# Performance work log

Hardware: AMD Instinct MI355X
Metric: run time of the kernel (lower is better)

Reference implementation:

```python
import jax, jax.numpy as jnp
import numpy as np

NEG_INF = -9e15  # matches torch's -9000000000000000.0 mask value
ALPHA = 0.2      # LeakyReLU negative slope


def setup_inputs() -> dict:
    key = jax.random.key(0)
    k1, k2, k3, k4 = jax.random.split(key, 4)
    B, N, Fin, Fout = 8, 2048, 256, 256
    h = jax.random.normal(k1, (B, N, Fin), dtype=jnp.float32)
    adj = jax.random.randint(k2, (B, N, N), 0, 2, dtype=jnp.int32)
    # xavier_uniform with gain=1.414
    limW = 1.414 * np.sqrt(6.0 / (Fin + Fout))
    W = jax.random.uniform(k3, (Fin, Fout), minval=-limW, maxval=limW, dtype=jnp.float32)
    lima = 1.414 * np.sqrt(6.0 / (2 * Fout + 1))
    a = jax.random.uniform(k4, (2 * Fout, 1), minval=-lima, maxval=lima, dtype=jnp.float32)
    return {"h": h, "adj": adj, "W": W, "a": a}


def reference(h, adj, W, a):
    # h: (B, N, Fin), adj: (B, N, N), W: (Fin, Fout), a: (2*Fout, 1)
    Fout = W.shape[1]
    Wh = jnp.einsum('bni,io->bno', h, W)                 # (B, N, Fout)
    # e[b,i,j] = leakyrelu(Wh[b,i] @ a1 + Wh[b,j] @ a2) -- equivalent to the
    # original concat([Wh_i, Wh_j]) @ a without the O(N^2 * 2F) intermediate.
    e1 = Wh @ a[:Fout, 0]                                # (B, N)
    e2 = Wh @ a[Fout:, 0]                                # (B, N)
    e = jax.nn.leaky_relu(e1[:, :, None] + e2[:, None, :], negative_slope=ALPHA)
    masked = jnp.where(adj > 0, e, NEG_INF)
    attention = jax.nn.softmax(masked, axis=-1)          # (B, N, N)
    # dropout omitted (deterministic eval-mode reference)
    h_prime = jnp.einsum('bij,bjo->bio', attention, Wh)  # (B, N, Fout)
    return jax.nn.elu(h_prime), attention
```

## Files before the change

### kernel.cpp

```cpp
#include <hip/hip_runtime.h>
#include <hip/hip_bf16.h>
#include <stdint.h>

#define NEG_INF -9.0e15f
#define LRELU_ALPHA 0.2f
#define LOG2E 1.442695040888963f

using bf16x8  = __attribute__((ext_vector_type(8))) short;
using f32x4   = __attribute__((ext_vector_type(4))) float;
using short4v = __attribute__((ext_vector_type(4))) short;
using int4v   = __attribute__((ext_vector_type(4))) int;
using float4v = __attribute__((ext_vector_type(4))) float;
using uint4v  = __attribute__((ext_vector_type(4))) unsigned;

static __device__ __forceinline__ float b2f(short s) {
  unsigned u = ((unsigned)(unsigned short)s) << 16;
  return __builtin_bit_cast(float, u);
}
static __device__ __forceinline__ short f2bf(float f) {
  unsigned u = __builtin_bit_cast(unsigned, f);
  u = u + 0x7FFFu + ((u >> 16) & 1u);
  return (short)(u >> 16);
}
static __device__ __forceinline__ unsigned cvtpk_bf16(float lo, float hi) {
  unsigned r;
  asm volatile("v_cvt_pk_bf16_f32 %0, %1, %2" : "=v"(r) : "v"(lo), "v"(hi));
  return r;
}
static __device__ __forceinline__ void gload16(const void* g, void* l) {
  __builtin_amdgcn_global_load_lds((const __attribute__((address_space(1))) void*)g,
                                   (__attribute__((address_space(3))) void*)l, 16, 0, 0);
}

__global__ __launch_bounds__(256) void castT_W_kernel(
    const float* __restrict__ src, short* __restrict__ dst)
{
  __shared__ float t[64][65];
  const int m0 = blockIdx.x * 64, n0 = blockIdx.y * 64;
  const int tid = threadIdx.x;
  const int rr = tid >> 3, cc = (tid & 7) * 8;
#pragma unroll
  for (int p = 0; p < 2; ++p) {
    int row = rr + p * 32;
    const float* sp = src + (m0 + row) * 256 + n0 + cc;
    float4v v0 = *(const float4v*)sp;
    float4v v1 = *(const float4v*)(sp + 4);
#pragma unroll
    for (int j = 0; j < 4; ++j) { t[row][cc + j] = v0[j]; t[row][cc + 4 + j] = v1[j]; }
  }
  __syncthreads();
#pragma unroll
  for (int p = 0; p < 2; ++p) {
    int orow = rr + p * 32;
    short vv[8] __attribute__((aligned(16)));
#pragma unroll
    for (int j = 0; j < 8; ++j) vv[j] = f2bf(t[cc + j][orow]);
    short* dp = dst + (n0 + orow) * 256 + m0 + cc;
    *(int4v*)dp = *(const int4v*)vv;
  }
}

__global__ __launch_bounds__(256) void transpose_bf16_kernel(
    const short* __restrict__ src, short* __restrict__ dst,
    int M, int N, long long ss, long long ds)
{
  __shared__ short t[64][68];
  const int b = blockIdx.z;
  src += (long long)b * ss; dst += (long long)b * ds;
  const int m0 = blockIdx.x * 64, n0 = blockIdx.y * 64;
  const int tid = threadIdx.x;
  const int rr = tid >> 3, cc = (tid & 7) * 8;
#pragma unroll
  for (int p = 0; p < 2; ++p) {
    int row = rr + p * 32;
    const short* sp = src + (long long)(m0 + row) * N + n0 + cc;
    short4v v0 = *(const short4v*)sp;
    short4v v1 = *(const short4v*)(sp + 4);
    *(short4v*)&t[row][cc]     = v0;
    *(short4v*)&t[row][cc + 4] = v1;
  }
  __syncthreads();
#pragma unroll
  for (int p = 0; p < 2; ++p) {
    int orow = rr + p * 32;
    short vv[8] __attribute__((aligned(16)));
#pragma unroll
    for (int j = 0; j < 8; ++j) vv[j] = t[cc + j][orow];
    short* dp = dst + (long long)(n0 + orow) * M + m0 + cc;
    *(int4v*)dp = *(const int4v*)vv;
  }
}

__global__ __launch_bounds__(256) void evec_kernel(
    const short* __restrict__ Wh, const float* __restrict__ a,
    float* __restrict__ e1, float* __restrict__ e2)
{
  const int wid = threadIdx.x >> 6, lane = threadIdx.x & 63;
  const long long r = (long long)blockIdx.x * 4 + wid;
  short4v hv   = *(const short4v*)(Wh + r * 256 + lane * 4);
  float4v a1v  = *(const float4v*)(a + lane * 4);
  float4v a2v  = *(const float4v*)(a + 256 + lane * 4);
  float s1 = 0.f, s2 = 0.f;
#pragma unroll
  for (int k = 0; k < 4; ++k) {
    float x = b2f(hv[k]);
    s1 += x * a1v[k];
    s2 += x * a2v[k];
  }
#pragma unroll
  for (int off = 32; off > 0; off >>= 1) {
    s1 += __shfl_xor(s1, off, 64);
    s2 += __shfl_xor(s2, off, 64);
  }
  if (lane == 0) { e1[r] = s1; e2[r] = s2; }
}

__global__ __launch_bounds__(256) void pack_stats_kernel(
    const int* __restrict__ adj, const float* __restrict__ e1,
    const float* __restrict__ e2, unsigned char* __restrict__ mask,
    float* __restrict__ Lr, float* __restrict__ Dr)
{
  const int i = blockIdx.x;
  const int b = blockIdx.y;
  const long long row = (long long)b * 2048 + i;
  const int tid = threadIdx.x;
  const int wid = tid >> 6, lane = tid & 63;
  const int j0 = tid * 8;

  const int*   arow = adj + row * 2048 + j0;
  const float  ei   = e1[row];
  const float* e2b  = e2 + b * 2048 + j0;

  int4v   a0 = *(const int4v*)(arow);
  int4v   a1 = *(const int4v*)(arow + 4);
  float4v f0 = *(const float4v*)(e2b);
  float4v f1 = *(const float4v*)(e2b + 4);

  float s[8]; unsigned byte = 0u;
#pragma unroll
  for (int k = 0; k < 8; ++k) {
    float x = ei + (k < 4 ? f0[k] : f1[k - 4]);
    float v = fmaxf(x, LRELU_ALPHA * x);
    int  ad = (k < 4 ? a0[k] : a1[k - 4]);
    if (ad > 0) { s[k] = v; byte |= (1u << k); } else s[k] = NEG_INF;
  }
  float m = s[0];
#pragma unroll
  for (int k = 1; k < 8; ++k) m = fmaxf(m, s[k]);
#pragma unroll
  for (int off = 32; off > 0; off >>= 1) m = fmaxf(m, __shfl_xor(m, off, 64));

  __shared__ float wmax[4], wsum[4];
  if (lane == 0) wmax[wid] = m;
  __syncthreads();
  const float M = fmaxf(fmaxf(wmax[0], wmax[1]), fmaxf(wmax[2], wmax[3]));
  const bool empty = (M == NEG_INF);

  mask[row * 256 + tid] = empty ? (unsigned char)0xFF : (unsigned char)byte;

  float t = 0.f;
#pragma unroll
  for (int k = 0; k < 8; ++k) t += __expf(s[k] - M);
#pragma unroll
  for (int off = 32; off > 0; off >>= 1) t += __shfl_xor(t, off, 64);
  if (lane == 0) wsum[wid] = t;
  __syncthreads();
  if (tid == 0) {
    const float S = wsum[0] + wsum[1] + wsum[2] + wsum[3];
    Lr[row] = empty ? 0.0f : LOG2E;
    Dr[row] = empty ? -11.0f : (-M * LOG2E - __log2f(S));
  }
}

__global__ __launch_bounds__(256, 2) void pv_kernel(
    const unsigned char* __restrict__ mask, const float* __restrict__ e1,
    const float* __restrict__ e2, const float* __restrict__ Lr,
    const float* __restrict__ Dr, const short* __restrict__ Bt,
    float* __restrict__ attnw, float* __restrict__ C)
{
  __shared__ short As0[32 * 64],  As1[32 * 64];
  __shared__ short Bs0[256 * 64], Bs1[256 * 64];
  const int bid = blockIdx.x;
  const int bz  = bid & 7;
  const int M0  = (bid >> 3) << 5;
  const int tid = threadIdx.x;
  const int w = tid >> 6, lane = tid & 63;
  const int g = lane >> 4, lr = lane & 15;

  const long long rb = (long long)bz * 2048;
  Bt    += (long long)bz * 524288;
  attnw += (long long)bz * 4194304;
  C     += (long long)bz * 524288;

  const int pr = tid >> 3, kc8 = tid & 7;
  const int prow = M0 + pr;
  const float E1p = e1[rb + prow];
  const float Lp  = Lr[rb + prow];
  const float Dp  = Dr[rb + prow];
  const unsigned char* mrow = mask + (rb + prow) * 256;
  float* arow = attnw + (long long)prow * 2048;
  const int as_off = pr * 64 + ((kc8 ^ (pr & 7)) << 3);
  const float* e2b = e2 + rb;

  const int bcol_off = lane >> 3;
  const int bchunk   = (lane & 7) ^ ((lane >> 3) & 7);

  f32x4 acc[2][4] = {};

  auto STAGE = [&](short* BsD, short* AsD, int k0) {
#pragma unroll
    for (int q = 0; q < 8; ++q) {
      int pp = w * 8 + q;
      int col = pp * 8 + bcol_off;
      gload16(Bt + (long long)col * 2048 + k0 + bchunk * 8, BsD + pp * 512);
    }
    const unsigned by = mrow[(k0 >> 3) + kc8];
    const int kk = k0 + kc8 * 8;
    float4v eo = *(const float4v*)(e2b + kk);
    float4v eh = *(const float4v*)(e2b + kk + 4);
    float p[8];
#pragma unroll
    for (int e = 0; e < 8; ++e) {
      float x = E1p + (e < 4 ? eo[e] : eh[e - 4]);
      float v = fmaxf(x, LRELU_ALPHA * x);
      float P = __builtin_amdgcn_exp2f(fmaf(v, Lp, Dp));
      p[e] = ((by >> e) & 1u) ? P : 0.0f;
    }
    float4v o0, o1;
#pragma unroll
    for (int e = 0; e < 4; ++e) { o0[e] = p[e]; o1[e] = p[e + 4]; }
    *(float4v*)(arow + kk)     = o0;
    *(float4v*)(arow + kk + 4) = o1;
    uint4v uv;
    uv[0] = cvtpk_bf16(p[0], p[1]);
    uv[1] = cvtpk_bf16(p[2], p[3]);
    uv[2] = cvtpk_bf16(p[4], p[5]);
    uv[3] = cvtpk_bf16(p[6], p[7]);
    *(bf16x8*)(AsD + as_off) = __builtin_bit_cast(bf16x8, uv);
  };

  auto COMPUTE = [&](const short* BsD, const short* AsD) {
    bf16x8 af[2][2], bfr[4][2];
#pragma unroll
    for (int i = 0; i < 2; ++i) {
      int row = i * 16 + lr;
#pragma unroll
      for (int s = 0; s < 2; ++s)
        af[i][s] = *(const bf16x8*)(AsD + row * 64 + (((s * 4 + g) ^ (row & 7)) << 3));
    }
#pragma unroll
    for (int j = 0; j < 4; ++j) {
      int col = w * 64 + j * 16 + lr;
#pragma unroll
      for (int s = 0; s < 2; ++s)
        bfr[j][s] = *(const bf16x8*)(BsD + col * 64 + (((s * 4 + g) ^ (col & 7)) << 3));
    }
#pragma unroll
    for (int s = 0; s < 2; ++s)
#pragma unroll
      for (int i = 0; i < 2; ++i)
#pragma unroll
        for (int j = 0; j < 4; ++j)
          acc[i][j] = __builtin_amdgcn_mfma_f32_16x16x32_bf16(af[i][s], bfr[j][s], acc[i][j], 0, 0, 0);
  };

  STAGE(Bs0, As0, 0);
  __syncthreads();
  for (int t = 0; t < 32; t += 2) {
    STAGE(Bs1, As1, (t + 1) * 64);
    COMPUTE(Bs0, As0);
    __syncthreads();
    if (t + 2 < 32) STAGE(Bs0, As0, (t + 2) * 64);
    COMPUTE(Bs1, As1);
    __syncthreads();
  }

#pragma unroll
  for (int i = 0; i < 2; ++i) {
    int row_base = M0 + i * 16 + 4 * g;
#pragma unroll
    for (int j = 0; j < 4; ++j) {
      int col = w * 64 + j * 16 + lr;
#pragma unroll
      for (int r = 0; r < 4; ++r) {
        float v = acc[i][j][r];
        v = (v > 0.f) ? v : (__expf(v) - 1.f);
        C[(long long)(row_base + r) * 256 + col] = v;
      }
    }
  }
}

__global__ __launch_bounds__(256) void gemm_h_kernel(
    const float* __restrict__ A, const short* __restrict__ Bt,
    short* __restrict__ C, int N, int K)
{
  __shared__ short As[128 * 32];
  __shared__ short Bs[128 * 32];
  const int m0 = blockIdx.x * 128, n0 = blockIdx.y * 128;
  const int tid = threadIdx.x;
  const int w = tid >> 6, lane = tid & 63;
  const int wr = w >> 1, wc = w & 1;
  const int g = lane >> 4, lr = lane & 15;

  f32x4 acc[4][4] = {};

  for (int k0 = 0; k0 < K; k0 += 32) {
    __syncthreads();
#pragma unroll
    for (int q = 0; q < 2; ++q) {
      int c = q * 256 + tid;
      int row = c >> 2, kq = (c & 3) << 3;
      const float* ap = A + (long long)(m0 + row) * K + k0 + kq;
      float4v u0 = *(const float4v*)ap;
      float4v u1 = *(const float4v*)(ap + 4);
      uint4v uv;
      uv[0] = cvtpk_bf16(u0[0], u0[1]);
      uv[1] = cvtpk_bf16(u0[2], u0[3]);
      uv[2] = cvtpk_bf16(u1[0], u1[1]);
      uv[3] = cvtpk_bf16(u1[2], u1[3]);
      *(bf16x8*)(As + c * 8) = __builtin_bit_cast(bf16x8, uv);
    }
#pragma unroll
    for (int q = 0; q < 2; ++q) {
      int p = w * 2 + q;
      int c = p * 64 + lane;
      int row = c >> 2, kq = (c & 3) << 3;
      gload16(Bt + (long long)(n0 + row) * K + k0 + kq, Bs + p * 512);
    }
    __syncthreads();

    bf16x8 af[4], bfr[4];
#pragma unroll
    for (int i = 0; i < 4; ++i) {
      af[i]  = *(const bf16x8*)(As + (wr * 64 + i * 16 + lr) * 32 + 8 * g);
      bfr[i] = *(const bf16x8*)(Bs + (wc * 64 + i * 16 + lr) * 32 + 8 * g);
    }
#pragma unroll
    for (int i = 0; i < 4; ++i)
#pragma unroll
      for (int j = 0; j < 4; ++j)
        acc[i][j] = __builtin_amdgcn_mfma_f32_16x16x32_bf16(af[i], bfr[j], acc[i][j], 0, 0, 0);
  }

#pragma unroll
  for (int i = 0; i < 4; ++i) {
    int row_base = m0 + wr * 64 + i * 16 + 4 * g;
#pragma unroll
    for (int j = 0; j < 4; ++j) {
      int col = n0 + wc * 64 + j * 16 + lr;
#pragma unroll
      for (int r = 0; r < 4; ++r)
        C[(long long)(row_base + r) * N + col] = f2bf(acc[i][j][r]);
    }
  }
}

extern "C" void kernel_launch(void* const* d_in, const int* in_sizes, int n_in,
                              void* d_out, int out_size, void* d_ws, size_t ws_size,
                              hipStream_t stream)
{
  const float* h   = (const float*)d_in[0];
  const int*   adj = (const int*)d_in[1];
  const float* W   = (const float*)d_in[2];
  const float* a   = (const float*)d_in[3];

  float* hp_out   = (float*)d_out;
  float* attn_out = hp_out + 4194304LL;

  unsigned char* mask = (unsigned char*)d_ws;
  short* W_t  = (short*)(mask + 4194304);
  short* Wh   = W_t + 65536;
  short* Wh_t = Wh + 4194304;
  float* e1   = (float*)(Wh_t + 4194304);
  float* e2   = e1 + 16384;
  float* Lr   = e2 + 16384;
  float* Dr   = Lr + 16384;

  castT_W_kernel<<<dim3(4, 4), 256, 0, stream>>>(W, W_t);
  gemm_h_kernel<<<dim3(128, 2, 1), 256, 0, stream>>>(h, W_t, Wh, 256, 256);
  transpose_bf16_kernel<<<dim3(32, 4, 8), 256, 0, stream>>>(Wh, Wh_t, 2048, 256, 524288LL, 524288LL);
  evec_kernel<<<4096, 256, 0, stream>>>(Wh, a, e1, e2);
  pack_stats_kernel<<<dim3(2048, 8), 256, 0, stream>>>(adj, e1, e2, mask, Lr, Dr);
  pv_kernel<<<512, 256, 0, stream>>>(mask, e1, e2, Lr, Dr, Wh_t, attn_out, hp_out);
}
```

Before: 120.6 us.

## Fuse Wh transpose into GEMM epilogue, compute e-vectors from h·(W·a), shrink pv K-tile

Precomputes W·a1 and W·a2 in a combined prep kernel, so e1/e2 come straight from fp32 h instead of from the bf16 Wh. The GEMM now writes its output transposed through shared memory, which removes the separate transpose kernel and the row-major Wh buffer. The pv kernel's K tile is halved to 32 with a new swizzle and occupancy raised to 4 blocks per CU, trading more loop iterations and barriers for higher occupancy. Computing e1/e2 from fp32 h also changes their rounding slightly compared with the bf16 Wh path.

```diff
diff --git a/kernel.cpp b/kernel.cpp
--- a/kernel.cpp
+++ b/kernel.cpp
@@ -11,12 +11,9 @@
 using short4v = __attribute__((ext_vector_type(4))) short;
 using int4v   = __attribute__((ext_vector_type(4))) int;
 using float4v = __attribute__((ext_vector_type(4))) float;
+using uint2v  = __attribute__((ext_vector_type(2))) unsigned;
 using uint4v  = __attribute__((ext_vector_type(4))) unsigned;
 
-static __device__ __forceinline__ float b2f(short s) {
-  unsigned u = ((unsigned)(unsigned short)s) << 16;
-  return __builtin_bit_cast(float, u);
-}
 static __device__ __forceinline__ short f2bf(float f) {
   unsigned u = __builtin_bit_cast(unsigned, f);
   u = u + 0x7FFFu + ((u >> 16) & 1u);
@@ -32,81 +29,75 @@
                                    (__attribute__((address_space(3))) void*)l, 16, 0, 0);
 }
 
-__global__ __launch_bounds__(256) void castT_W_kernel(
-    const float* __restrict__ src, short* __restrict__ dst)
-{
-  __shared__ float t[64][65];
-  const int m0 = blockIdx.x * 64, n0 = blockIdx.y * 64;
+__global__ __launch_bounds__(256) void prep_kernel(
+    const float* __restrict__ W, const float* __restrict__ a,
+    short* __restrict__ W_t, float* __restrict__ aW1, float* __restrict__ aW2)
+{
+  const int bid = blockIdx.x;
   const int tid = threadIdx.x;
-  const int rr = tid >> 3, cc = (tid & 7) * 8;
-#pragma unroll
-  for (int p = 0; p < 2; ++p) {
-    int row = rr + p * 32;
-    const float* sp = src + (m0 + row) * 256 + n0 + cc;
-    float4v v0 = *(const float4v*)sp;
-    float4v v1 = *(const float4v*)(sp + 4);
-#pragma unroll
-    for (int j = 0; j < 4; ++j) { t[row][cc + j] = v0[j]; t[row][cc + 4 + j] = v1[j]; }
-  }
-  __syncthreads();
-#pragma unroll
-  for (int p = 0; p < 2; ++p) {
-    int orow = rr + p * 32;
-    short vv[8] __attribute__((aligned(16)));
-#pragma unroll
-    for (int j = 0; j < 8; ++j) vv[j] = f2bf(t[cc + j][orow]);
-    short* dp = dst + (n0 + orow) * 256 + m0 + cc;
-    *(int4v*)dp = *(const int4v*)vv;
-  }
-}
-
-__global__ __launch_bounds__(256) void transpose_bf16_kernel(
-    const short* __restrict__ src, short* __restrict__ dst,
-    int M, int N, long long ss, long long ds)
-{
-  __shared__ short t[64][68];
-  const int b = blockIdx.z;
-  src += (long long)b * ss; dst += (long long)b * ds;
-  const int m0 = blockIdx.x * 64, n0 = blockIdx.y * 64;
-  const int tid = threadIdx.x;
-  const int rr = tid >> 3, cc = (tid & 7) * 8;
-#pragma unroll
-  for (int p = 0; p < 2; ++p) {
-    int row = rr + p * 32;
-    const short* sp = src + (long long)(m0 + row) * N + n0 + cc;
-    short4v v0 = *(const short4v*)sp;
-    short4v v1 = *(const short4v*)(sp + 4);
-    *(short4v*)&t[row][cc]     = v0;
-    *(short4v*)&t[row][cc + 4] = v1;
-  }
-  __syncthreads();
-#pragma unroll
-  for (int p = 0; p < 2; ++p) {
-    int orow = rr + p * 32;
-    short vv[8] __attribute__((aligned(16)));
-#pragma unroll
-    for (int j = 0; j < 8; ++j) vv[j] = t[cc + j][orow];
-    short* dp = dst + (long long)(n0 + orow) * M + m0 + cc;
-    *(int4v*)dp = *(const int4v*)vv;
-  }
-}
-
-__global__ __launch_bounds__(256) void evec_kernel(
-    const short* __restrict__ Wh, const float* __restrict__ a,
-    float* __restrict__ e1, float* __restrict__ e2)
+  if (bid < 16) {
+    __shared__ float t[64][65];
+    const int m0 = (bid & 3) * 64, n0 = (bid >> 2) * 64;
+    const int rr = tid >> 3, cc = (tid & 7) * 8;
+#pragma unroll
+    for (int p = 0; p < 2; ++p) {
+      int row = rr + p * 32;
+      const float* sp = W + (m0 + row) * 256 + n0 + cc;
+      float4v v0 = *(const float4v*)sp;
+      float4v v1 = *(const float4v*)(sp + 4);
+#pragma unroll
+      for (int j = 0; j < 4; ++j) { t[row][cc + j] = v0[j]; t[row][cc + 4 + j] = v1[j]; }
+    }
+    __syncthreads();
+#pragma unroll
+    for (int p = 0; p < 2; ++p) {
+      int orow = rr + p * 32;
+      short vv[8] __attribute__((aligned(16)));
+#pragma unroll
+      for (int j = 0; j < 8; ++j) vv[j] = f2bf(t[cc + j][orow]);
+      short* dp = W_t + (n0 + orow) * 256 + m0 + cc;
+      *(int4v*)dp = *(const int4v*)vv;
+    }
+  } else {
+    const int r8 = tid >> 3, o4 = (tid & 7) * 4;
+    float s1[8] = {}, s2[8] = {};
+#pragma unroll
+    for (int rp = 0; rp < 8; ++rp) {
+      int row = r8 + rp * 32;
+#pragma unroll
+      for (int k = 0; k < 8; ++k) {
+        int o = o4 + k * 32;
+        float4v wv = *(const float4v*)(W + row * 256 + o);
+        float4v a1 = *(const float4v*)(a + o);
+        float4v a2 = *(const float4v*)(a + 256 + o);
+#pragma unroll
+        for (int e = 0; e < 4; ++e) { s1[rp] += wv[e] * a1[e]; s2[rp] += wv[e] * a2[e]; }
+      }
+    }
+#pragma unroll
+    for (int rp = 0; rp < 8; ++rp) {
+#pragma unroll
+      for (int off = 4; off > 0; off >>= 1) {
+        s1[rp] += __shfl_xor(s1[rp], off, 64);
+        s2[rp] += __shfl_xor(s2[rp], off, 64);
+      }
+      if ((tid & 7) == 0) { aW1[r8 + rp * 32] = s1[rp]; aW2[r8 + rp * 32] = s2[rp]; }
+    }
+  }
+}
+
+__global__ __launch_bounds__(256) void evec2_kernel(
+    const float* __restrict__ h, const float* __restrict__ aW1,
+    const float* __restrict__ aW2, float* __restrict__ e1, float* __restrict__ e2)
 {
   const int wid = threadIdx.x >> 6, lane = threadIdx.x & 63;
   const long long r = (long long)blockIdx.x * 4 + wid;
-  short4v hv   = *(const short4v*)(Wh + r * 256 + lane * 4);
-  float4v a1v  = *(const float4v*)(a + lane * 4);
-  float4v a2v  = *(const float4v*)(a + 256 + lane * 4);
+  float4v hv  = *(const float4v*)(h + r * 256 + lane * 4);
+  float4v a1v = *(const float4v*)(aW1 + lane * 4);
+  float4v a2v = *(const float4v*)(aW2 + lane * 4);
   float s1 = 0.f, s2 = 0.f;
 #pragma unroll
-  for (int k = 0; k < 4; ++k) {
-    float x = b2f(hv[k]);
-    s1 += x * a1v[k];
-    s2 += x * a2v[k];
-  }
+  for (int k = 0; k < 4; ++k) { s1 += hv[k] * a1v[k]; s2 += hv[k] * a2v[k]; }
 #pragma unroll
   for (int off = 32; off > 0; off >>= 1) {
     s1 += __shfl_xor(s1, off, 64);
@@ -115,188 +106,13 @@
   if (lane == 0) { e1[r] = s1; e2[r] = s2; }
 }
 
-__global__ __launch_bounds__(256) void pack_stats_kernel(
-    const int* __restrict__ adj, const float* __restrict__ e1,
-    const float* __restrict__ e2, unsigned char* __restrict__ mask,
-    float* __restrict__ Lr, float* __restrict__ Dr)
-{
-  const int i = blockIdx.x;
-  const int b = blockIdx.y;
-  const long long row = (long long)b * 2048 + i;
-  const int tid = threadIdx.x;
-  const int wid = tid >> 6, lane = tid & 63;
-  const int j0 = tid * 8;
-
-  const int*   arow = adj + row * 2048 + j0;
-  const float  ei   = e1[row];
-  const float* e2b  = e2 + b * 2048 + j0;
-
-  int4v   a0 = *(const int4v*)(arow);
-  int4v   a1 = *(const int4v*)(arow + 4);
-  float4v f0 = *(const float4v*)(e2b);
-  float4v f1 = *(const float4v*)(e2b + 4);
-
-  float s[8]; unsigned byte = 0u;
-#pragma unroll
-  for (int k = 0; k < 8; ++k) {
-    float x = ei + (k < 4 ? f0[k] : f1[k - 4]);
-    float v = fmaxf(x, LRELU_ALPHA * x);
-    int  ad = (k < 4 ? a0[k] : a1[k - 4]);
-    if (ad > 0) { s[k] = v; byte |= (1u << k); } else s[k] = NEG_INF;
-  }
-  float m = s[0];
-#pragma unroll
-  for (int k = 1; k < 8; ++k) m = fmaxf(m, s[k]);
-#pragma unroll
-  for (int off = 32; off > 0; off >>= 1) m = fmaxf(m, __shfl_xor(m, off, 64));
-
-  __shared__ float wmax[4], wsum[4];
-  if (lane == 0) wmax[wid] = m;
-  __syncthreads();
-  const float M = fmaxf(fmaxf(wmax[0], wmax[1]), fmaxf(wmax[2], wmax[3]));
-  const bool empty = (M == NEG_INF);
-
-  mask[row * 256 + tid] = empty ? (unsigned char)0xFF : (unsigned char)byte;
-
-  float t = 0.f;
-#pragma unroll
-  for (int k = 0; k < 8; ++k) t += __expf(s[k] - M);
-#pragma unroll
-  for (int off = 32; off > 0; off >>= 1) t += __shfl_xor(t, off, 64);
-  if (lane == 0) wsum[wid] = t;
-  __syncthreads();
-  if (tid == 0) {
-    const float S = wsum[0] + wsum[1] + wsum[2] + wsum[3];
-    Lr[row] = empty ? 0.0f : LOG2E;
-    Dr[row] = empty ? -11.0f : (-M * LOG2E - __log2f(S));
-  }
-}
-
-__global__ __launch_bounds__(256, 2) void pv_kernel(
-    const unsigned char* __restrict__ mask, const float* __restrict__ e1,
-    const float* __restrict__ e2, const float* __restrict__ Lr,
-    const float* __restrict__ Dr, const short* __restrict__ Bt,
-    float* __restrict__ attnw, float* __restrict__ C)
-{
-  __shared__ short As0[32 * 64],  As1[32 * 64];
-  __shared__ short Bs0[256 * 64], Bs1[256 * 64];
-  const int bid = blockIdx.x;
-  const int bz  = bid & 7;
-  const int M0  = (bid >> 3) << 5;
-  const int tid = threadIdx.x;
-  const int w = tid >> 6, lane = tid & 63;
-  const int g = lane >> 4, lr = lane & 15;
-
-  const long long rb = (long long)bz * 2048;
-  Bt    += (long long)bz * 524288;
-  attnw += (long long)bz * 4194304;
-  C     += (long long)bz * 524288;
-
-  const int pr = tid >> 3, kc8 = tid & 7;
-  const int prow = M0 + pr;
-  const float E1p = e1[rb + prow];
-  const float Lp  = Lr[rb + prow];
-  const float Dp  = Dr[rb + prow];
-  const unsigned char* mrow = mask + (rb + prow) * 256;
-  float* arow = attnw + (long long)prow * 2048;
-  const int as_off = pr * 64 + ((kc8 ^ (pr & 7)) << 3);
-  const float* e2b = e2 + rb;
-
-  const int bcol_off = lane >> 3;
-  const int bchunk   = (lane & 7) ^ ((lane >> 3) & 7);
-
-  f32x4 acc[2][4] = {};
-
-  auto STAGE = [&](short* BsD, short* AsD, int k0) {
-#pragma unroll
-    for (int q = 0; q < 8; ++q) {
-      int pp = w * 8 + q;
-      int col = pp * 8 + bcol_off;
-      gload16(Bt + (long long)col * 2048 + k0 + bchunk * 8, BsD + pp * 512);
-    }
-    const unsigned by = mrow[(k0 >> 3) + kc8];
-    const int kk = k0 + kc8 * 8;
-    float4v eo = *(const float4v*)(e2b + kk);
-    float4v eh = *(const float4v*)(e2b + kk + 4);
-    float p[8];
-#pragma unroll
-    for (int e = 0; e < 8; ++e) {
-      float x = E1p + (e < 4 ? eo[e] : eh[e - 4]);
-      float v = fmaxf(x, LRELU_ALPHA * x);
-      float P = __builtin_amdgcn_exp2f(fmaf(v, Lp, Dp));
-      p[e] = ((by >> e) & 1u) ? P : 0.0f;
-    }
-    float4v o0, o1;
-#pragma unroll
-    for (int e = 0; e < 4; ++e) { o0[e] = p[e]; o1[e] = p[e + 4]; }
-    *(float4v*)(arow + kk)     = o0;
-    *(float4v*)(arow + kk + 4) = o1;
-    uint4v uv;
-    uv[0] = cvtpk_bf16(p[0], p[1]);
-    uv[1] = cvtpk_bf16(p[2], p[3]);
-    uv[2] = cvtpk_bf16(p[4], p[5]);
-    uv[3] = cvtpk_bf16(p[6], p[7]);
-    *(bf16x8*)(AsD + as_off) = __builtin_bit_cast(bf16x8, uv);
-  };
-
-  auto COMPUTE = [&](const short* BsD, const short* AsD) {
-    bf16x8 af[2][2], bfr[4][2];
-#pragma unroll
-    for (int i = 0; i < 2; ++i) {
-      int row = i * 16 + lr;
-#pragma unroll
-      for (int s = 0; s < 2; ++s)
-        af[i][s] = *(const bf16x8*)(AsD + row * 64 + (((s * 4 + g) ^ (row & 7)) << 3));
-    }
-#pragma unroll
-    for (int j = 0; j < 4; ++j) {
-      int col = w * 64 + j * 16 + lr;
-#pragma unroll
-      for (int s = 0; s < 2; ++s)
-        bfr[j][s] = *(const bf16x8*)(BsD + col * 64 + (((s * 4 + g) ^ (col & 7)) << 3));
-    }
-#pragma unroll
-    for (int s = 0; s < 2; ++s)
-#pragma unroll
-      for (int i = 0; i < 2; ++i)
-#pragma unroll
-        for (int j = 0; j < 4; ++j)
-          acc[i][j] = __builtin_amdgcn_mfma_f32_16x16x32_bf16(af[i][s], bfr[j][s], acc[i][j], 0, 0, 0);
-  };
-
-  STAGE(Bs0, As0, 0);
-  __syncthreads();
-  for (int t = 0; t < 32; t += 2) {
-    STAGE(Bs1, As1, (t + 1) * 64);
-    COMPUTE(Bs0, As0);
-    __syncthreads();
-    if (t + 2 < 32) STAGE(Bs0, As0, (t + 2) * 64);
-    COMPUTE(Bs1, As1);
-    __syncthreads();
-  }
-
-#pragma unroll
-  for (int i = 0; i < 2; ++i) {
-    int row_base = M0 + i * 16 + 4 * g;
-#pragma unroll
-    for (int j = 0; j < 4; ++j) {
-      int col = w * 64 + j * 16 + lr;
-#pragma unroll
-      for (int r = 0; r < 4; ++r) {
-        float v = acc[i][j][r];
-        v = (v > 0.f) ? v : (__expf(v) - 1.f);
-        C[(long long)(row_base + r) * 256 + col] = v;
-      }
-    }
-  }
-}
-
 __global__ __launch_bounds__(256) void gemm_h_kernel(
     const float* __restrict__ A, const short* __restrict__ Bt,
-    short* __restrict__ C, int N, int K)
+    short* __restrict__ Wht)
 {
   __shared__ short As[128 * 32];
   __shared__ short Bs[128 * 32];
+  __shared__ short T[128][136];
   const int m0 = blockIdx.x * 128, n0 = blockIdx.y * 128;
   const int tid = threadIdx.x;
   const int w = tid >> 6, lane = tid & 63;
@@ -305,13 +121,13 @@
 
   f32x4 acc[4][4] = {};
 
-  for (int k0 = 0; k0 < K; k0 += 32) {
+  for (int k0 = 0; k0 < 256; k0 += 32) {
     __syncthreads();
 #pragma unroll
     for (int q = 0; q < 2; ++q) {
       int c = q * 256 + tid;
       int row = c >> 2, kq = (c & 3) << 3;
-      const float* ap = A + (long long)(m0 + row) * K + k0 + kq;
+      const float* ap = A + (long long)(m0 + row) * 256 + k0 + kq;
       float4v u0 = *(const float4v*)ap;
       float4v u1 = *(const float4v*)(ap + 4);
       uint4v uv;
@@ -326,7 +142,7 @@
       int p = w * 2 + q;
       int c = p * 64 + lane;
       int row = c >> 2, kq = (c & 3) << 3;
-      gload16(Bt + (long long)(n0 + row) * K + k0 + kq, Bs + p * 512);
+      gload16(Bt + (long long)(n0 + row) * 256 + k0 + kq, Bs + p * 512);
     }
     __syncthreads();
 
@@ -343,15 +159,193 @@
         acc[i][j] = __builtin_amdgcn_mfma_f32_16x16x32_bf16(af[i], bfr[j], acc[i][j], 0, 0, 0);
   }
 
+  __syncthreads();
 #pragma unroll
   for (int i = 0; i < 4; ++i) {
-    int row_base = m0 + wr * 64 + i * 16 + 4 * g;
+    int row_base = wr * 64 + i * 16 + 4 * g;
 #pragma unroll
     for (int j = 0; j < 4; ++j) {
-      int col = n0 + wc * 64 + j * 16 + lr;
+      int col = wc * 64 + j * 16 + lr;
 #pragma unroll
       for (int r = 0; r < 4; ++r)
-        C[(long long)(row_base + r) * N + col] = f2bf(acc[i][j][r]);
+        T[col][row_base + r] = f2bf(acc[i][j][r]);
+    }
+  }
+  __syncthreads();
+  const int b = m0 >> 11, mloc = m0 & 2047;
+  short* wb = Wht + (long long)b * 524288 + mloc;
+#pragma unroll
+  for (int p = 0; p < 8; ++p) {
+    int c = (tid >> 4) + p * 16;
+    int off = (tid & 15) * 8;
+    bf16x8 v = *(const bf16x8*)(&T[c][off]);
+    *(bf16x8*)(wb + (long long)(n0 + c) * 2048 + off) = v;
+  }
+}
+
+__global__ __launch_bounds__(256) void pack_stats_kernel(
+    const int* __restrict__ adj, const float* __restrict__ e1,
+    const float* __restrict__ e2, unsigned char* __restrict__ mask,
+    float* __restrict__ Lr, float* __restrict__ Dr)
+{
+  const int i = blockIdx.x;
+  const int b = blockIdx.y;
+  const long long row = (long long)b * 2048 + i;
+  const int tid = threadIdx.x;
+  const int wid = tid >> 6, lane = tid & 63;
+  const int j0 = tid * 8;
+
+  const int*   arow = adj + row * 2048 + j0;
+  const float  ei   = e1[row];
+  const float* e2b  = e2 + b * 2048 + j0;
+
+  int4v   a0 = *(const int4v*)(arow);
+  int4v   a1 = *(const int4v*)(arow + 4);
+  float4v f0 = *(const float4v*)(e2b);
+  float4v f1 = *(const float4v*)(e2b + 4);
+
+  float s[8]; unsigned byte = 0u;
+#pragma unroll
+  for (int k = 0; k < 8; ++k) {
+    float x = ei + (k < 4 ? f0[k] : f1[k - 4]);
+    float v = fmaxf(x, LRELU_ALPHA * x);
+    int  ad = (k < 4 ? a0[k] : a1[k - 4]);
+    if (ad > 0) { s[k] = v; byte |= (1u << k); } else s[k] = NEG_INF;
+  }
+  float m = s[0];
+#pragma unroll
+  for (int k = 1; k < 8; ++k) m = fmaxf(m, s[k]);
+#pragma unroll
+  for (int off = 32; off > 0; off >>= 1) m = fmaxf(m, __shfl_xor(m, off, 64));
+
+  __shared__ float wmax[4], wsum[4];
+  if (lane == 0) wmax[wid] = m;
+  __syncthreads();
+  const float M = fmaxf(fmaxf(wmax[0], wmax[1]), fmaxf(wmax[2], wmax[3]));
+  const bool empty = (M == NEG_INF);
+
+  mask[row * 256 + tid] = empty ? (unsigned char)0xFF : (unsigned char)byte;
+
+  float t = 0.f;
+#pragma unroll
+  for (int k = 0; k < 8; ++k) t += __expf(s[k] - M);
+#pragma unroll
+  for (int off = 32; off > 0; off >>= 1) t += __shfl_xor(t, off, 64);
+  if (lane == 0) wsum[wid] = t;
+  __syncthreads();
+  if (tid == 0) {
+    const float S = wsum[0] + wsum[1] + wsum[2] + wsum[3];
+    Lr[row] = empty ? 0.0f : LOG2E;
+    Dr[row] = empty ? -11.0f : (-M * LOG2E - __log2f(S));
+  }
+}
+
+__global__ __launch_bounds__(256, 4) void pv_kernel(
+    const unsigned char* __restrict__ mask, const float* __restrict__ e1,
+    const float* __restrict__ e2, const float* __restrict__ Lr,
+    const float* __restrict__ Dr, const short* __restrict__ Bt,
+    float* __restrict__ attnw, float* __restrict__ C)
+{
+  __shared__ short As0[32 * 32],  As1[32 * 32];
+  __shared__ short Bs0[256 * 32], Bs1[256 * 32];
+  const int bid = blockIdx.x;
+  const int bz  = bid & 7;
+  const int M0  = (bid >> 3) << 5;
+  const int tid = threadIdx.x;
+  const int w = tid >> 6, lane = tid & 63;
+  const int g = lane >> 4, lr = lane & 15;
+
+  const long long rb = (long long)bz * 2048;
+  Bt    += (long long)bz * 524288;
+  attnw += (long long)bz * 4194304;
+  C     += (long long)bz * 524288;
+
+  const int pr = tid >> 3, k4 = (tid & 7) << 2;
+  const int prow = M0 + pr;
+  const float E1p = e1[rb + prow];
+  const float Lp  = Lr[rb + prow];
+  const float Dp  = Dr[rb + prow];
+  const unsigned char* mrow = mask + (rb + prow) * 256;
+  float* arow = attnw + (long long)prow * 2048;
+  const int kc = k4 >> 3;
+  const int as_off = pr * 32 + ((kc ^ ((pr >> 1) & 3)) << 3) + (k4 & 7);
+  const float* e2b = e2 + rb;
+
+  const int bcol_off = lane >> 2;
+  const int bchunk   = (lane & 3) ^ ((lane >> 3) & 3);
+
+  f32x4 acc[2][4] = {};
+
+  auto STAGE = [&](short* BsD, short* AsD, int k0) {
+#pragma unroll
+    for (int q = 0; q < 4; ++q) {
+      int pp = w * 4 + q;
+      int col = pp * 16 + bcol_off;
+      gload16(Bt + (long long)col * 2048 + k0 + bchunk * 8, BsD + pp * 512);
+    }
+    const unsigned by = (unsigned)(mrow[(k0 + k4) >> 3] >> (k4 & 7)) & 0xFu;
+    const int kk = k0 + k4;
+    float4v ev = *(const float4v*)(e2b + kk);
+    float p4[4];
+#pragma unroll
+    for (int e = 0; e < 4; ++e) {
+      float x = E1p + ev[e];
+      float v = fmaxf(x, LRELU_ALPHA * x);
+      float P = __builtin_amdgcn_exp2f(fmaf(v, Lp, Dp));
+      p4[e] = ((by >> e) & 1u) ? P : 0.0f;
+    }
+    float4v o;
+#pragma unroll
+    for (int e = 0; e < 4; ++e) o[e] = p4[e];
+    *(float4v*)(arow + kk) = o;
+    uint2v uv;
+    uv[0] = cvtpk_bf16(p4[0], p4[1]);
+    uv[1] = cvtpk_bf16(p4[2], p4[3]);
+    *(uint2v*)(AsD + as_off) = uv;
+  };
+
+  auto COMPUTE = [&](const short* BsD, const short* AsD) {
+    bf16x8 af[2], bfr[4];
+#pragma unroll
+    for (int i = 0; i < 2; ++i) {
+      int row = i * 16 + lr;
+      af[i] = *(const bf16x8*)(AsD + row * 32 + ((g ^ ((row >> 1) & 3)) << 3));
+    }
+#pragma unroll
+    for (int j = 0; j < 4; ++j) {
+      int col = w * 64 + j * 16 + lr;
+      bfr[j] = *(const bf16x8*)(BsD + col * 32 + ((g ^ ((col >> 1) & 3)) << 3));
+    }
+#pragma unroll
+    for (int i = 0; i < 2; ++i)
+#pragma unroll
+      for (int j = 0; j < 4; ++j)
+        acc[i][j] = __builtin_amdgcn_mfma_f32_16x16x32_bf16(af[i], bfr[j], acc[i][j], 0, 0, 0);
+  };
+
+  STAGE(Bs0, As0, 0);
+  __syncthreads();
+  for (int t = 0; t < 64; t += 2) {
+    STAGE(Bs1, As1, (t + 1) * 32);
+    COMPUTE(Bs0, As0);
+    __syncthreads();
+    if (t + 2 < 64) STAGE(Bs0, As0, (t + 2) * 32);
+    COMPUTE(Bs1, As1);
+    __syncthreads();
+  }
+
+#pragma unroll
+  for (int i = 0; i < 2; ++i) {
+    int row_base = M0 + i * 16 + 4 * g;
+#pragma unroll
+    for (int j = 0; j < 4; ++j) {
+      int col = w * 64 + j * 16 + lr;
+#pragma unroll
+      for (int r = 0; r < 4; ++r) {
+        float v = acc[i][j][r];
+        v = (v > 0.f) ? v : (__expf(v) - 1.f);
+        C[(long long)(row_base + r) * 256 + col] = v;
+      }
     }
   }
 }
@@ -370,17 +364,17 @@
 
   unsigned char* mask = (unsigned char*)d_ws;
   short* W_t  = (short*)(mask + 4194304);
-  short* Wh   = W_t + 65536;
-  short* Wh_t = Wh + 4194304;
+  short* Wh_t = W_t + 65536;
   float* e1   = (float*)(Wh_t + 4194304);
   float* e2   = e1 + 16384;
   float* Lr   = e2 + 16384;
   float* Dr   = Lr + 16384;
-
-  castT_W_kernel<<<dim3(4, 4), 256, 0, stream>>>(W, W_t);
-  gemm_h_kernel<<<dim3(128, 2, 1), 256, 0, stream>>>(h, W_t, Wh, 256, 256);
-  transpose_bf16_kernel<<<dim3(32, 4, 8), 256, 0, stream>>>(Wh, Wh_t, 2048, 256, 524288LL, 524288LL);
-  evec_kernel<<<4096, 256, 0, stream>>>(Wh, a, e1, e2);
+  float* aW1  = Dr + 16384;
+  float* aW2  = aW1 + 256;
+
+  prep_kernel<<<17, 256, 0, stream>>>(W, a, W_t, aW1, aW2);
+  evec2_kernel<<<4096, 256, 0, stream>>>(h, aW1, aW2, e1, e2);
+  gemm_h_kernel<<<dim3(128, 2), 256, 0, stream>>>(h, W_t, Wh_t);
   pack_stats_kernel<<<dim3(2048, 8), 256, 0, stream>>>(adj, e1, e2, mask, Lr, Dr);
   pv_kernel<<<512, 256, 0, stream>>>(mask, e1, e2, Lr, Dr, Wh_t, attn_out, hp_out);
 }
```

New measurement: 123.0 us. About the same (+2.0%).
